# Kernel tuning notes

Measured on AMD Instinct MI355X. Metric: run time of the kernel, lower is better.

The kernel has to match this reference:

```python
import jax, jax.numpy as jnp
import numpy as np

N_NODES = 50000
N_EDGES = 300000
F_IN = 11
D = 256


def _gcn_conv(h, src, dst, deg_inv_sqrt, W, b, n):
    """PyG GCNConv: out = D^{-1/2} (A + I) D^{-1/2} (h W) + b.
    src/dst already include self-loops; deg_inv_sqrt precomputed."""
    norm = deg_inv_sqrt[src] * deg_inv_sqrt[dst]          # [E+N]
    hw = h @ W                                            # [N, D]
    msg = hw[src] * norm[:, None]                         # [E+N, D]
    out = jax.ops.segment_sum(msg, dst, num_segments=n)   # [N, D]
    return out + b


def setup_inputs() -> dict:
    key = jax.random.key(0)
    ks = jax.random.split(key, 8)
    x = jax.random.normal(ks[0], (N_NODES, F_IN), dtype=jnp.float32)
    edge_index = jax.random.randint(ks[1], (2, N_EDGES), 0, N_NODES, dtype=jnp.int32)
    s = 0.05
    W_embed = jax.random.normal(ks[2], (F_IN, D), dtype=jnp.float32) * s
    b_embed = jnp.zeros((D,), dtype=jnp.float32)
    W1 = jax.random.normal(ks[3], (D, D), dtype=jnp.float32) * s
    b1 = jnp.zeros((D,), dtype=jnp.float32)
    W2 = jax.random.normal(ks[4], (D, D), dtype=jnp.float32) * s
    b2 = jnp.zeros((D,), dtype=jnp.float32)
    return {"x": x, "edge_index": edge_index, "W_embed": W_embed, "b_embed": b_embed,
            "W1": W1, "b1": b1, "W2": W2, "b2": b2}


def reference(x, edge_index, W_embed, b_embed, W1, b1, W2, b2):
    n = x.shape[0]
    # add self-loops (PyG GCNConv default add_self_loops=True)
    loop = jnp.arange(n, dtype=edge_index.dtype)
    src = jnp.concatenate([edge_index[0], loop])
    dst = jnp.concatenate([edge_index[1], loop])
    # symmetric normalization: deg over target index with unit edge weights
    deg = jax.ops.segment_sum(jnp.ones(src.shape, dtype=x.dtype), dst, num_segments=n)
    deg_inv_sqrt = jnp.where(deg > 0, jax.lax.rsqrt(jnp.maximum(deg, 1e-12)), 0.0)

    h = jax.nn.relu(x @ W_embed + b_embed)                # embed + relu
    h = jax.nn.relu(_gcn_conv(h, src, dst, deg_inv_sqrt, W1, b1, n))
    h = _gcn_conv(h, src, dst, deg_inv_sqrt, W2, b2, n)
    return h
```

## Files before the change

kernel.cpp:

```cpp
#include <hip/hip_runtime.h>

#define N_NODES 50000
#define N_EDGES 300000
#define N_TOT   350000
#define D       256
#define MPAD    50048
#define SCAN_B  196
#define BLKM    64
#define LGRID   (MPAD / BLKM)
#define EMAX    896

typedef __attribute__((ext_vector_type(8))) short bf16x8;
typedef __attribute__((ext_vector_type(4))) float f32x4;
typedef __attribute__((ext_vector_type(8))) unsigned short u16x8;
typedef __attribute__((ext_vector_type(4))) unsigned short u16x4;

__device__ __forceinline__ float bf2f(unsigned short b) {
    union { unsigned u; float f; } v; v.u = ((unsigned)b) << 16; return v.f;
}
__device__ __forceinline__ unsigned short f2bf(float f) {
    union { float f; unsigned u; } v; v.f = f;
    unsigned u = v.u;
    unsigned r = (u + 0x7FFFu + ((u >> 16) & 1u)) >> 16;
    return (unsigned short)r;
}

__global__ __launch_bounds__(256) void k1_kernel(
        const float* __restrict__ x, const int* __restrict__ ei,
        const float* __restrict__ We, const float* __restrict__ be,
        const float* __restrict__ W1, const float* __restrict__ W2,
        int* __restrict__ cnt,
        unsigned short* __restrict__ Wt1, unsigned short* __restrict__ Wt2,
        unsigned short* __restrict__ hA) {
    int t = threadIdx.x, b = blockIdx.x;
    int tid = b * 256 + t;

    if (tid < N_TOT) {
        int dst = (tid < N_EDGES) ? ei[N_EDGES + tid] : (tid - N_EDGES);
        atomicAdd(&cnt[dst], 1);
    }
    if (tid < 2 * D * D) {
        int wsel = tid >> 16, rem = tid & 65535;
        int tt = rem >> 8, bb = rem & 255;
        const float* W = wsel ? W2 : W1;
        unsigned short* Wt = wsel ? Wt2 : Wt1;
        Wt[bb * D + tt] = f2bf(W[tt * D + bb]);
    }
    float w[11];
    #pragma unroll
    for (int k = 0; k < 11; ++k) w[k] = We[k * D + t];
    float bb = be[t];
    #pragma unroll
    for (int ni = 0; ni < 8; ++ni) {
        int node = b * 8 + ni;
        float acc = 0.f;
        if (node < N_NODES) {
            acc = bb;
            #pragma unroll
            for (int k = 0; k < 11; ++k) acc += x[node * 11 + k] * w[k];
            acc = fmaxf(acc, 0.f);
        }
        hA[(size_t)node * D + t] = f2bf(acc);
    }
}

__global__ __launch_bounds__(256) void k2_kernel(const int* __restrict__ cnt,
                                                 float* __restrict__ dis,
                                                 int* __restrict__ locs,
                                                 int* __restrict__ bsum,
                                                 int* __restrict__ done) {
    __shared__ int ws[4];
    __shared__ int amLast;
    int t = threadIdx.x;
    int lane = t & 63, wv4 = t >> 6;
    int i = blockIdx.x * 256 + t;
    int v = (i < N_NODES) ? cnt[i] : 0;
    if (i < N_NODES) dis[i] = rsqrtf((float)v);
    int s = v;
    #pragma unroll
    for (int d = 1; d < 64; d <<= 1) {
        int u = __shfl_up(s, d, 64);
        if (lane >= d) s += u;
    }
    if (lane == 63) ws[wv4] = s;
    __syncthreads();
    int off = 0;
    #pragma unroll
    for (int k = 0; k < 4; ++k) if (k < wv4) off += ws[k];
    s += off;
    if (i < N_NODES) locs[i] = s;
    if (t == 255) {
        bsum[blockIdx.x] = s;
        __threadfence();
        amLast = (atomicAdd(done, 1) == SCAN_B - 1);
    }
    __syncthreads();
    if (amLast) {
        __threadfence();
        int vv = 0;
        if (t < SCAN_B)
            vv = __hip_atomic_load(&bsum[t], __ATOMIC_RELAXED, __HIP_MEMORY_SCOPE_AGENT);
        int ss = vv;
        #pragma unroll
        for (int d = 1; d < 64; d <<= 1) {
            int u = __shfl_up(ss, d, 64);
            if (lane >= d) ss += u;
        }
        __syncthreads();
        if (lane == 63) ws[wv4] = ss;
        __syncthreads();
        int off2 = 0;
        #pragma unroll
        for (int k = 0; k < 4; ++k) if (k < wv4) off2 += ws[k];
        ss += off2;
        if (t < SCAN_B) bsum[t] = ss - vv;
    }
}

__global__ __launch_bounds__(256) void k3_kernel(const int* __restrict__ ei,
                          const int* __restrict__ locs,
                          const int* __restrict__ bsum, const float* __restrict__ dis,
                          int* __restrict__ fc, int* __restrict__ rowptr,
                          int2* __restrict__ epk) {
    int tid = blockIdx.x * 256 + threadIdx.x;
    if (tid == 0) rowptr[0] = 0;
    if (tid < N_NODES)
        rowptr[tid + 1] = locs[tid] + bsum[tid >> 8];
    if (tid < N_TOT) {
        int src, dst;
        if (tid < N_EDGES) { src = ei[tid]; dst = ei[N_EDGES + tid]; }
        else               { src = dst = tid - N_EDGES; }
        int base = bsum[dst >> 8] + ((dst & 255) ? locs[dst - 1] : 0);
        int pos = base + atomicAdd(&fc[dst], 1);
        epk[pos] = make_int2(src, __float_as_int(dis[src] * dis[dst]));
    }
}

__global__ __launch_bounds__(256, 4) void layer_kernel(
        const unsigned short* __restrict__ hw,
        const int* __restrict__ rowptr,
        const int2* __restrict__ epk,
        const unsigned short* __restrict__ Bt,
        const float* __restrict__ bias,
        unsigned short* __restrict__ out_bf,
        float* __restrict__ out_f32,
        int mode) {
    __shared__ unsigned short lA[BLKM * D];
    __shared__ int2 eL[EMAX];
    __shared__ int rL[BLKM + 1];
    int t = threadIdx.x;
    int bid = blockIdx.x;
    int wid = t >> 6, lane = t & 63;
    int h = lane >> 5, hl = lane & 31;
    int hw8 = wid * 2 + h;
    int m0 = bid * BLKM;
    int mEnd = m0 + BLKM; if (mEnd > N_NODES) mEnd = N_NODES;

    int s0b = rowptr[m0];
    int s1b = rowptr[mEnd];
    int nE = s1b - s0b;
    bool useL = (nE <= EMAX);
    if (t <= BLKM) {
        int idx = m0 + t;
        rL[t] = rowptr[idx > N_NODES ? N_NODES : idx];
    }
    if (useL)
        for (int i = t; i < nE; i += 256) eL[i] = epk[s0b + i];
    __syncthreads();

    for (int j = 0; j < 8; ++j) {
        int nn = hw8 * 8 + j;
        int s0 = rL[nn], s1 = rL[nn + 1];
        int deg = s1 - s0;
        int ls0 = s0 - s0b;
        float acc[8] = {};
        for (int off = 0; off < deg; off += 8) {
            int se[8]; float ne[8];
            #pragma unroll
            for (int e = 0; e < 8; ++e) {
                int idx = off + e;
                int2 ep = make_int2(0, 0);
                if (idx < deg) ep = useL ? eL[ls0 + idx] : epk[s0 + idx];
                se[e] = ep.x; ne[e] = __int_as_float(ep.y);
            }
            u16x8 rw[8];
            #pragma unroll
            for (int e = 0; e < 8; ++e)
                rw[e] = *(const u16x8*)(hw + (size_t)se[e] * D + hl * 8);
            #pragma unroll
            for (int e = 0; e < 8; ++e)
                #pragma unroll
                for (int k = 0; k < 8; ++k) acc[k] += ne[e] * bf2f(rw[e][k]);
        }
        u16x8 o;
        #pragma unroll
        for (int k = 0; k < 8; ++k) o[k] = f2bf(acc[k]);
        int chunk = (hl & ~7) | ((hl ^ nn) & 7);
        *(u16x8*)(lA + nn * D + chunk * 8) = o;
    }

    __syncthreads();

    int q = lane >> 4, r = lane & 15;
    int noff = wid * 64;
    const unsigned short* Bw = Bt + (size_t)(noff + r) * D + q * 8;
    f32x4 acc4[4][4] = {};
    #pragma unroll 1
    for (int st = 0; st < 8; ++st) {
        bf16x8 af[4], bfr[4];
        #pragma unroll
        for (int nt = 0; nt < 4; ++nt)
            bfr[nt] = *(const bf16x8*)(Bw + (size_t)(nt * 16) * D + st * 32);
        #pragma unroll
        for (int mt = 0; mt < 4; ++mt) {
            int row = mt * 16 + r;
            int ch = st * 4 + q;
            int chs = (ch & ~7) | ((ch ^ row) & 7);
            af[mt] = *(const bf16x8*)(lA + row * D + chs * 8);
        }
        #pragma unroll
        for (int mt = 0; mt < 4; ++mt)
            #pragma unroll
            for (int nt = 0; nt < 4; ++nt)
                acc4[mt][nt] = __builtin_amdgcn_mfma_f32_16x16x32_bf16(
                    bfr[nt], af[mt], acc4[mt][nt], 0, 0, 0);
    }

    #pragma unroll
    for (int mt = 0; mt < 4; ++mt) {
        int mrow = m0 + mt * 16 + r;
        if (mrow >= N_NODES) continue;
        #pragma unroll
        for (int nt = 0; nt < 4; ++nt) {
            int col = noff + nt * 16 + (q << 2);
            float4 bv = *(const float4*)(bias + col);
            float v[4] = { acc4[mt][nt][0] + bv.x, acc4[mt][nt][1] + bv.y,
                           acc4[mt][nt][2] + bv.z, acc4[mt][nt][3] + bv.w };
            if (mode) {
                u16x4 o;
                #pragma unroll
                for (int i = 0; i < 4; ++i) o[i] = f2bf(fmaxf(v[i], 0.f));
                *(u16x4*)(out_bf + (size_t)mrow * D + col) = o;
            } else {
                float4 o = { v[0], v[1], v[2], v[3] };
                *(float4*)(out_f32 + (size_t)mrow * D + col) = o;
            }
        }
    }
}

extern "C" void kernel_launch(void* const* d_in, const int* in_sizes, int n_in,
                              void* d_out, int out_size, void* d_ws, size_t ws_size,
                              hipStream_t stream) {
    const float* x  = (const float*)d_in[0];
    const int*   ei = (const int*)d_in[1];
    const float* We = (const float*)d_in[2];
    const float* be = (const float*)d_in[3];
    const float* W1 = (const float*)d_in[4];
    const float* b1 = (const float*)d_in[5];
    const float* W2 = (const float*)d_in[6];
    const float* b2 = (const float*)d_in[7];
    float* out = (float*)d_out;

    char* w = (char*)d_ws;
    auto alloc = [&](size_t bytes) {
        char* p = w;
        w += (bytes + 255) & ~(size_t)255;
        return p;
    };
    int*            cnt    = (int*)alloc((size_t)N_NODES * 4);
    int*            fc     = (int*)alloc((size_t)N_NODES * 4);
    int*            done   = (int*)alloc(4);
    size_t zero_span = (size_t)((char*)(done + 64) - (char*)cnt);
    int*            rowptr = (int*)alloc((size_t)(N_NODES + 1) * 4);
    int*            locs   = (int*)alloc((size_t)N_NODES * 4);
    int*            bsum   = (int*)alloc((size_t)SCAN_B * 4);
    float*          dis    = (float*)alloc((size_t)N_NODES * 4);
    int2*           epk    = (int2*)alloc((size_t)N_TOT * 8);
    unsigned short* Wt1    = (unsigned short*)alloc((size_t)D * D * 2);
    unsigned short* Wt2    = (unsigned short*)alloc((size_t)D * D * 2);
    unsigned short* hA     = (unsigned short*)alloc((size_t)MPAD * D * 2);
    unsigned short* h1     = (unsigned short*)alloc((size_t)MPAD * D * 2);

    hipMemsetAsync(cnt, 0, zero_span, stream);
    k1_kernel<<<MPAD / 8, 256, 0, stream>>>(x, ei, We, be, W1, W2, cnt, Wt1, Wt2, hA);
    k2_kernel<<<SCAN_B, 256, 0, stream>>>(cnt, dis, locs, bsum, done);
    k3_kernel<<<(N_TOT + 255) / 256, 256, 0, stream>>>(ei, locs, bsum, dis, fc,
                                                       rowptr, epk);
    layer_kernel<<<LGRID, 256, 0, stream>>>(hA, rowptr, epk, Wt1, b1,
                                            h1, nullptr, 1);
    layer_kernel<<<LGRID, 256, 0, stream>>>(h1, rowptr, epk, Wt2, b2,
                                            nullptr, out, 0);
}
```

Measured before the change: 235.4 us.

## Split fused layer into column-grouped aggregation and standalone LDS-staged GEMM

Each fused aggregate-then-GEMM layer kernel becomes two kernels. A sparse aggregation kernel splits the 256 feature columns into 8 groups of 32, one group per block. It computes edge norms on the fly from dis and stores edge sources as 16-bit indices. A separate 128x128 MFMA GEMM kernel then reads the aggregated features, staging A and B through LDS with direct global-to-LDS loads and an XCD-aware block mapping. The aim is to shrink edge metadata traffic, raise parallelism and improve L2 locality in the gather. The cost is an extra round-trip of the intermediate through global memory and two more launches.

```diff
diff --git a/kernel.cpp b/kernel.cpp
--- a/kernel.cpp
+++ b/kernel.cpp
@@ -6,8 +6,9 @@
 #define D       256
 #define MPAD    50048
 #define SCAN_B  196
-#define BLKM    64
-#define LGRID   (MPAD / BLKM)
+#define TILE    64
+#define AGRID   (MPAD / TILE * 8)
+#define GEMM_B  784
 #define EMAX    896
 
 typedef __attribute__((ext_vector_type(8))) short bf16x8;
@@ -23,6 +24,11 @@
     unsigned u = v.u;
     unsigned r = (u + 0x7FFFu + ((u >> 16) & 1u)) >> 16;
     return (unsigned short)r;
+}
+__device__ __forceinline__ void g2lds16(const unsigned short* g, unsigned short* l) {
+    __builtin_amdgcn_global_load_lds(
+        (const __attribute__((address_space(1))) void*)g,
+        (__attribute__((address_space(3))) void*)l, 16, 0, 0);
 }
 
 __global__ __launch_bounds__(256) void k1_kernel(
@@ -119,9 +125,9 @@
 
 __global__ __launch_bounds__(256) void k3_kernel(const int* __restrict__ ei,
                           const int* __restrict__ locs,
-                          const int* __restrict__ bsum, const float* __restrict__ dis,
+                          const int* __restrict__ bsum,
                           int* __restrict__ fc, int* __restrict__ rowptr,
-                          int2* __restrict__ epk) {
+                          unsigned short* __restrict__ esrc) {
     int tid = blockIdx.x * 256 + threadIdx.x;
     if (tid == 0) rowptr[0] = 0;
     if (tid < N_NODES)
@@ -132,118 +138,153 @@
         else               { src = dst = tid - N_EDGES; }
         int base = bsum[dst >> 8] + ((dst & 255) ? locs[dst - 1] : 0);
         int pos = base + atomicAdd(&fc[dst], 1);
-        epk[pos] = make_int2(src, __float_as_int(dis[src] * dis[dst]));
-    }
-}
-
-__global__ __launch_bounds__(256, 4) void layer_kernel(
+        esrc[pos] = (unsigned short)src;
+    }
+}
+
+__global__ __launch_bounds__(256) void aggk(
         const unsigned short* __restrict__ hw,
         const int* __restrict__ rowptr,
-        const int2* __restrict__ epk,
-        const unsigned short* __restrict__ Bt,
-        const float* __restrict__ bias,
-        unsigned short* __restrict__ out_bf,
-        float* __restrict__ out_f32,
-        int mode) {
-    __shared__ unsigned short lA[BLKM * D];
-    __shared__ int2 eL[EMAX];
-    __shared__ int rL[BLKM + 1];
-    int t = threadIdx.x;
-    int bid = blockIdx.x;
+        const unsigned short* __restrict__ esrc,
+        const float* __restrict__ dis,
+        unsigned short* __restrict__ gA) {
+    __shared__ unsigned short sL[EMAX];
+    __shared__ int rL[TILE + 1];
+    int t = threadIdx.x, bid = blockIdx.x;
+    int cg = bid & 7, tile = bid >> 3;
+    int m0 = tile * TILE;
+    int mEnd = m0 + TILE; if (mEnd > N_NODES) mEnd = N_NODES;
+
+    int s0b = rowptr[m0], s1b = rowptr[mEnd];
+    int nE = s1b - s0b;
+    bool useL = (nE <= EMAX);
+    if (t <= TILE) {
+        int idx = m0 + t;
+        rL[t] = rowptr[idx > N_NODES ? N_NODES : idx];
+    }
+    if (useL)
+        for (int i = t; i < nE; i += 256) sL[i] = esrc[s0b + i];
+    __syncthreads();
+
     int wid = t >> 6, lane = t & 63;
     int h = lane >> 5, hl = lane & 31;
     int hw8 = wid * 2 + h;
-    int m0 = bid * BLKM;
-    int mEnd = m0 + BLKM; if (mEnd > N_NODES) mEnd = N_NODES;
-
-    int s0b = rowptr[m0];
-    int s1b = rowptr[mEnd];
-    int nE = s1b - s0b;
-    bool useL = (nE <= EMAX);
-    if (t <= BLKM) {
-        int idx = m0 + t;
-        rL[t] = rowptr[idx > N_NODES ? N_NODES : idx];
-    }
-    if (useL)
-        for (int i = t; i < nE; i += 256) eL[i] = epk[s0b + i];
-    __syncthreads();
+    int g = hl >> 3, c = hl & 7;
+    const unsigned short* tb = hw + cg * 32 + c * 4;
 
     for (int j = 0; j < 8; ++j) {
         int nn = hw8 * 8 + j;
-        int s0 = rL[nn], s1 = rL[nn + 1];
-        int deg = s1 - s0;
+        int node = m0 + nn;
+        int s0 = rL[nn], deg = rL[nn + 1] - s0;
         int ls0 = s0 - s0b;
-        float acc[8] = {};
+        float disD = (deg > 0) ? dis[node] : 0.f;
+        float a0 = 0.f, a1 = 0.f, a2 = 0.f, a3 = 0.f;
         for (int off = 0; off < deg; off += 8) {
-            int se[8]; float ne[8];
+            int i1 = off + g, i2 = off + 4 + g;
+            int src1 = 0, src2 = 0; float n1 = 0.f, n2 = 0.f;
+            if (i1 < deg) {
+                src1 = useL ? sL[ls0 + i1] : esrc[s0 + i1];
+                n1 = dis[src1] * disD;
+            }
+            if (i2 < deg) {
+                src2 = useL ? sL[ls0 + i2] : esrc[s0 + i2];
+                n2 = dis[src2] * disD;
+            }
+            u16x4 r1 = *(const u16x4*)(tb + (size_t)src1 * D);
+            u16x4 r2 = *(const u16x4*)(tb + (size_t)src2 * D);
+            a0 += n1 * bf2f(r1[0]); a1 += n1 * bf2f(r1[1]);
+            a2 += n1 * bf2f(r1[2]); a3 += n1 * bf2f(r1[3]);
+            a0 += n2 * bf2f(r2[0]); a1 += n2 * bf2f(r2[1]);
+            a2 += n2 * bf2f(r2[2]); a3 += n2 * bf2f(r2[3]);
+        }
+        a0 += __shfl_xor(a0, 8, 64);  a1 += __shfl_xor(a1, 8, 64);
+        a2 += __shfl_xor(a2, 8, 64);  a3 += __shfl_xor(a3, 8, 64);
+        a0 += __shfl_xor(a0, 16, 64); a1 += __shfl_xor(a1, 16, 64);
+        a2 += __shfl_xor(a2, 16, 64); a3 += __shfl_xor(a3, 16, 64);
+        if (hl < 8) {
+            u16x4 o = { f2bf(a0), f2bf(a1), f2bf(a2), f2bf(a3) };
+            *(u16x4*)(gA + (size_t)node * D + cg * 32 + hl * 4) = o;
+        }
+    }
+}
+
+__global__ __launch_bounds__(256) void gemm_kernel(const unsigned short* __restrict__ A,
+                                                   const unsigned short* __restrict__ Bt,
+                                                   const float* __restrict__ bias,
+                                                   unsigned short* __restrict__ Cb,
+                                                   float* __restrict__ Cf,
+                                                   int mode) {
+    __shared__ unsigned short lA[128 * 64];
+    __shared__ unsigned short lB[128 * 64];
+    int t = threadIdx.x;
+    int bid = blockIdx.x;
+
+    int xcd = bid & 7, s = bid >> 3;
+    int pair = xcd * 49 + (s >> 1);
+    int ny   = s & 1;
+    if (pair >= MPAD / 128) return;
+
+    int wv = t >> 6, lane = t & 63;
+    int m0 = pair * 128;
+    int n0 = ny * 128;
+    int moff = (wv & 1) * 64, noff = (wv >> 1) * 64;
+    int q = lane >> 4, r = lane & 15;
+
+    int srow[4], scol[4];
+    #pragma unroll
+    for (int j = 0; j < 4; ++j) {
+        int idx = j * 256 + t;
+        srow[j] = idx >> 3;
+        scol[j] = ((idx & 7) ^ (srow[j] & 7)) * 8;
+    }
+
+    f32x4 acc[4][4] = {};
+    for (int kk = 0; kk < D; kk += 64) {
+        __syncthreads();
+        #pragma unroll
+        for (int j = 0; j < 4; ++j) {
+            int idx = j * 256 + t;
+            g2lds16(A  + (size_t)(m0 + srow[j]) * D + kk + scol[j], lA + idx * 8);
+            g2lds16(Bt + (size_t)(n0 + srow[j]) * D + kk + scol[j], lB + idx * 8);
+        }
+        __syncthreads();
+        #pragma unroll
+        for (int ks = 0; ks < 2; ++ks) {
+            bf16x8 a[4], b[4];
             #pragma unroll
-            for (int e = 0; e < 8; ++e) {
-                int idx = off + e;
-                int2 ep = make_int2(0, 0);
-                if (idx < deg) ep = useL ? eL[ls0 + idx] : epk[s0 + idx];
-                se[e] = ep.x; ne[e] = __int_as_float(ep.y);
-            }
-            u16x8 rw[8];
+            for (int mt = 0; mt < 4; ++mt) {
+                int row = moff + mt * 16 + r;
+                a[mt] = *(const bf16x8*)(lA + row * 64 + (((ks * 4 + q) ^ (r & 7)) * 8));
+            }
             #pragma unroll
-            for (int e = 0; e < 8; ++e)
-                rw[e] = *(const u16x8*)(hw + (size_t)se[e] * D + hl * 8);
+            for (int nt = 0; nt < 4; ++nt) {
+                int row = noff + nt * 16 + r;
+                b[nt] = *(const bf16x8*)(lB + row * 64 + (((ks * 4 + q) ^ (r & 7)) * 8));
+            }
             #pragma unroll
-            for (int e = 0; e < 8; ++e)
+            for (int mt = 0; mt < 4; ++mt)
                 #pragma unroll
-                for (int k = 0; k < 8; ++k) acc[k] += ne[e] * bf2f(rw[e][k]);
-        }
-        u16x8 o;
-        #pragma unroll
-        for (int k = 0; k < 8; ++k) o[k] = f2bf(acc[k]);
-        int chunk = (hl & ~7) | ((hl ^ nn) & 7);
-        *(u16x8*)(lA + nn * D + chunk * 8) = o;
-    }
-
-    __syncthreads();
-
-    int q = lane >> 4, r = lane & 15;
-    int noff = wid * 64;
-    const unsigned short* Bw = Bt + (size_t)(noff + r) * D + q * 8;
-    f32x4 acc4[4][4] = {};
-    #pragma unroll 1
-    for (int st = 0; st < 8; ++st) {
-        bf16x8 af[4], bfr[4];
-        #pragma unroll
-        for (int nt = 0; nt < 4; ++nt)
-            bfr[nt] = *(const bf16x8*)(Bw + (size_t)(nt * 16) * D + st * 32);
-        #pragma unroll
-        for (int mt = 0; mt < 4; ++mt) {
-            int row = mt * 16 + r;
-            int ch = st * 4 + q;
-            int chs = (ch & ~7) | ((ch ^ row) & 7);
-            af[mt] = *(const bf16x8*)(lA + row * D + chs * 8);
-        }
-        #pragma unroll
-        for (int mt = 0; mt < 4; ++mt)
-            #pragma unroll
-            for (int nt = 0; nt < 4; ++nt)
-                acc4[mt][nt] = __builtin_amdgcn_mfma_f32_16x16x32_bf16(
-                    bfr[nt], af[mt], acc4[mt][nt], 0, 0, 0);
-    }
-
+                for (int nt = 0; nt < 4; ++nt)
+                    acc[mt][nt] = __builtin_amdgcn_mfma_f32_16x16x32_bf16(b[nt], a[mt], acc[mt][nt], 0, 0, 0);
+        }
+    }
     #pragma unroll
     for (int mt = 0; mt < 4; ++mt) {
-        int mrow = m0 + mt * 16 + r;
-        if (mrow >= N_NODES) continue;
+        int mrow = m0 + moff + mt * 16 + r;
         #pragma unroll
         for (int nt = 0; nt < 4; ++nt) {
-            int col = noff + nt * 16 + (q << 2);
-            float4 bv = *(const float4*)(bias + col);
-            float v[4] = { acc4[mt][nt][0] + bv.x, acc4[mt][nt][1] + bv.y,
-                           acc4[mt][nt][2] + bv.z, acc4[mt][nt][3] + bv.w };
+            int ncol = n0 + noff + nt * 16 + (q << 2);
+            float4 bv = *(const float4*)(bias + ncol);
+            float v[4] = { acc[mt][nt][0] + bv.x, acc[mt][nt][1] + bv.y,
+                           acc[mt][nt][2] + bv.z, acc[mt][nt][3] + bv.w };
             if (mode) {
                 u16x4 o;
                 #pragma unroll
                 for (int i = 0; i < 4; ++i) o[i] = f2bf(fmaxf(v[i], 0.f));
-                *(u16x4*)(out_bf + (size_t)mrow * D + col) = o;
-            } else {
+                *(u16x4*)(Cb + (size_t)mrow * D + ncol) = o;
+            } else if (mrow < N_NODES) {
                 float4 o = { v[0], v[1], v[2], v[3] };
-                *(float4*)(out_f32 + (size_t)mrow * D + col) = o;
+                *(float4*)(Cf + (size_t)mrow * D + ncol) = o;
             }
         }
     }
@@ -276,19 +317,20 @@
     int*            locs   = (int*)alloc((size_t)N_NODES * 4);
     int*            bsum   = (int*)alloc((size_t)SCAN_B * 4);
     float*          dis    = (float*)alloc((size_t)N_NODES * 4);
-    int2*           epk    = (int2*)alloc((size_t)N_TOT * 8);
+    unsigned short* esrc   = (unsigned short*)alloc((size_t)N_TOT * 2);
     unsigned short* Wt1    = (unsigned short*)alloc((size_t)D * D * 2);
     unsigned short* Wt2    = (unsigned short*)alloc((size_t)D * D * 2);
     unsigned short* hA     = (unsigned short*)alloc((size_t)MPAD * D * 2);
     unsigned short* h1     = (unsigned short*)alloc((size_t)MPAD * D * 2);
+    unsigned short* gA     = (unsigned short*)alloc((size_t)MPAD * D * 2);
 
     hipMemsetAsync(cnt, 0, zero_span, stream);
     k1_kernel<<<MPAD / 8, 256, 0, stream>>>(x, ei, We, be, W1, W2, cnt, Wt1, Wt2, hA);
     k2_kernel<<<SCAN_B, 256, 0, stream>>>(cnt, dis, locs, bsum, done);
-    k3_kernel<<<(N_TOT + 255) / 256, 256, 0, stream>>>(ei, locs, bsum, dis, fc,
-                                                       rowptr, epk);
-    layer_kernel<<<LGRID, 256, 0, stream>>>(hA, rowptr, epk, Wt1, b1,
-                                            h1, nullptr, 1);
-    layer_kernel<<<LGRID, 256, 0, stream>>>(h1, rowptr, epk, Wt2, b2,
-                                            nullptr, out, 0);
-}
+    k3_kernel<<<(N_TOT + 255) / 256, 256, 0, stream>>>(ei, locs, bsum, fc,
+                                                       rowptr, esrc);
+    aggk<<<AGRID, 256, 0, stream>>>(hA, rowptr, esrc, dis, gA);
+    gemm_kernel<<<GEMM_B, 256, 0, stream>>>(gA, Wt1, b1, h1, nullptr, 1);
+    aggk<<<AGRID, 256, 0, stream>>>(h1, rowptr, esrc, dis, gA);
+    gemm_kernel<<<GEMM_B, 256, 0, stream>>>(gA, Wt2, b2, nullptr, out, 0);
+}
```

Result: slower. 306.8 us (+30.3%).
